# Kernel optimization log

Hardware: AMD Instinct MI355X
Metric: run time of the kernel (lower is better)

Reference implementation:

```python
import jax, jax.numpy as jnp
import numpy as np

# module config (init_kwargs + opts)
C = 64
RADIUS = 1.5          # radius in pixels
SIZE = 256            # square image size
K = 8                 # points_per_pixel (z-buffer depth)
RAD_POW = 2
TAU = 1.0


def setup_inputs() -> dict:
    key = jax.random.key(0)
    k1, k2 = jax.random.split(key)
    B, P = 2, 1024
    u = jax.random.uniform(k1, (B, P, 3), dtype=jnp.float32)
    xy = u[..., :2] * 2.0 - 1.0          # NDC xy in [-1, 1]
    z = u[..., 2:] * 1.9 + 0.1           # depth in [0.1, 2.0], in front of camera
    pts3D = jnp.concatenate([xy, z], axis=-1)
    src = jax.random.normal(k2, (B, C, P), dtype=jnp.float32)
    return {"pts3D": pts3D, "src": src}


def reference(pts3D, src):
    """Point rasterization (pytorch3d rasterize_points semantics for a square
    NDC image) + alpha-composite z-buffer blending, as in SynSin's
    RasterizePointsXYsBlending.forward (3-D src branch, alphacomposite)."""
    B, P, _ = pts3D.shape
    H = W = SIZE
    # module negates x and y before rasterizing (pytorch3d NDC: +x left, +y up)
    x = -pts3D[..., 0]                   # [B, P]
    y = -pts3D[..., 1]                   # [B, P]
    z = pts3D[..., 2]                    # [B, P]
    r_ndc = RADIUS / SIZE * 2.0          # radius in NDC units

    # pixel-center NDC coordinates
    xf = 1.0 - (2.0 * jnp.arange(W, dtype=pts3D.dtype) + 1.0) / W   # [W]
    yf = 1.0 - (2.0 * jnp.arange(H, dtype=pts3D.dtype) + 1.0) / H   # [H]

    dx2 = (xf[None, :, None] - x[:, None, :]) ** 2   # [B, W, P]
    dy2 = (yf[None, :, None] - y[:, None, :]) ** 2   # [B, H, P]
    dist2 = dy2[:, :, None, :] + dx2[:, None, :, :]  # [B, H, W, P] screen-space sq dist

    # a point covers a pixel if within radius and in front of the camera
    valid = (dist2 <= r_ndc * r_ndc) & (z[:, None, None, :] > 0.0)
    zkey = jnp.where(valid, z[:, None, None, :], jnp.inf)
    negz, idx = jax.lax.top_k(-zkey, K)              # K nearest in z, front-to-back
    sel_valid = jnp.isfinite(negz)                   # [B, H, W, K] (idx = -1 slots)

    dist_sel = jnp.take_along_axis(dist2, idx, axis=-1)   # [B, H, W, K]
    dist_n = dist_sel / (r_ndc ** RAD_POW)
    alphas = (1.0 - jnp.sqrt(jnp.clip(dist_n, 0.001, 1.0))) ** TAU
    alphas = jnp.where(sel_valid, alphas, 0.0)            # [B, H, W, K]

    # alpha compositing: w_k = a_k * prod_{j<k} (1 - a_j)
    one_m = 1.0 - alphas
    excl = jnp.concatenate(
        [jnp.ones_like(one_m[..., :1]), jnp.cumprod(one_m, axis=-1)[..., :-1]],
        axis=-1,
    )
    w = alphas * excl                                      # [B, H, W, K]

    feats = jnp.transpose(src, (0, 2, 1))                  # [B, P, C]
    idx_c = jnp.clip(idx, 0, P - 1).reshape(B, -1)         # [B, H*W*K]
    gathered = jnp.take_along_axis(feats, idx_c[..., None], axis=1)
    gathered = gathered.reshape(B, H, W, K, C)             # [B, H, W, K, C]

    out = jnp.einsum('bhwk,bhwkc->bchw', w, gathered)      # [B, C, H, W]
    return out
```

## Files before the change

kernel.cpp:

```cpp
#include <hip/hip_runtime.h>

#define NCH 64
#define IMG 256
#define KSEL 8
#define CAP 64
#define FPAD 17

__global__ __launch_bounds__(256) void raster_blend_kernel(
    const float* __restrict__ pts3D,
    const float* __restrict__ src,
    float* __restrict__ out,
    int P)
{
    const int h = blockIdx.x;
    const int b = blockIdx.y;
    const int w = threadIdx.x;
    const int HW = IMG * IMG;

    const float r_ndc  = (1.5f / (float)IMG) * 2.0f;
    const float r2     = r_ndc * r_ndc;
    const float inv_r2 = 1.0f / r2;

    const float yf = 1.0f - (2.0f * (float)h + 1.0f) / (float)IMG;
    const float xf = 1.0f - (2.0f * (float)w + 1.0f) / (float)IMG;

    __shared__ __align__(16) float4 cand[CAP];
    __shared__ int   cnt;
    __shared__ __align__(16) float featS[CAP * FPAD * 4];
    if (w == 0) cnt = 0;
    __syncthreads();

    const float* pb = pts3D + (size_t)b * P * 3;
    for (int p = w; p < P; p += 256) {
        float px = -pb[p * 3 + 0];
        float py = -pb[p * 3 + 1];
        float pz =  pb[p * 3 + 2];
        float dy = yf - py;
        if (dy * dy <= r2 && pz > 0.0f) {
            int slot = atomicAdd(&cnt, 1);
            if (slot < CAP)
                cand[slot] = make_float4(px, py, pz, __int_as_float(p));
        }
    }
    __syncthreads();
    const int n = min(cnt, CAP);

    const int myj = w >> 6;
    const int c   = w & 63;
    const float* sb = src + (size_t)b * NCH * P;
    int cidx[CAP / 4];
#pragma unroll
    for (int r = 0; r < CAP / 4; ++r) {
        int j = r * 4 + myj;
        if (j < n) cidx[r] = __float_as_int(cand[j].w);
    }
    float freg[CAP / 4];
#pragma unroll
    for (int r = 0; r < CAP / 4; ++r) {
        int j = r * 4 + myj;
        if (j < n) freg[r] = sb[(size_t)c * P + cidx[r]];
    }

    const float SENT = 1e30f;
    float zb[KSEL], db[KSEL];
    int   jb[KSEL];
#pragma unroll
    for (int s = 0; s < KSEL; ++s) { zb[s] = SENT; db[s] = 0.0f; jb[s] = 0; }

    for (int j = 0; j < n; ++j) {
        float4 e = cand[j];
        float dx = xf - e.x;
        float dy = yf - e.y;
        float d2 = fmaf(dx, dx, dy * dy);
        float z  = e.z;
        if (d2 <= r2 && z < zb[KSEL - 1]) {
            float carz = z, card = d2;
            int   carj = j;
#pragma unroll
            for (int s = 0; s < KSEL; ++s) {
                if (carz < zb[s]) {
                    float tz = zb[s]; zb[s] = carz; carz = tz;
                    float td = db[s]; db[s] = card; card = td;
                    int   tj = jb[s]; jb[s] = carj; carj = tj;
                }
            }
        }
    }

    float wk[KSEL];
    bool  vk[KSEL];
    float T = 1.0f;
#pragma unroll
    for (int s = 0; s < KSEL; ++s) {
        bool valid = zb[s] < 1e29f;
        vk[s] = valid;
        float dn = db[s] * inv_r2;
        dn = fminf(fmaxf(dn, 0.001f), 1.0f);
        float a = 1.0f - sqrtf(dn);
        a = valid ? a : 0.0f;
        wk[s] = a * T;
        T *= (1.0f - a);
    }

#pragma unroll
    for (int r = 0; r < CAP / 4; ++r) {
        int j = r * 4 + myj;
        if (j < n) featS[j * (FPAD * 4) + c] = freg[r];
    }
    __syncthreads();

    float4 acc[NCH / 4];
#pragma unroll
    for (int c4 = 0; c4 < NCH / 4; ++c4) acc[c4] = make_float4(0.f, 0.f, 0.f, 0.f);

    const float4* fv = (const float4*)featS;
#pragma unroll
    for (int k = 0; k < KSEL; ++k) {
        if (__any(vk[k])) {
            float wv = wk[k];
            const float4* fp = fv + jb[k] * FPAD;
#pragma unroll
            for (int c4 = 0; c4 < NCH / 4; ++c4) {
                float4 f = fp[c4];
                acc[c4].x = fmaf(wv, f.x, acc[c4].x);
                acc[c4].y = fmaf(wv, f.y, acc[c4].y);
                acc[c4].z = fmaf(wv, f.z, acc[c4].z);
                acc[c4].w = fmaf(wv, f.w, acc[c4].w);
            }
        }
    }

    float* op = out + (size_t)b * NCH * HW + (size_t)h * IMG + w;
#pragma unroll
    for (int c4 = 0; c4 < NCH / 4; ++c4) {
        op[(size_t)(4 * c4 + 0) * HW] = acc[c4].x;
        op[(size_t)(4 * c4 + 1) * HW] = acc[c4].y;
        op[(size_t)(4 * c4 + 2) * HW] = acc[c4].z;
        op[(size_t)(4 * c4 + 3) * HW] = acc[c4].w;
    }
}

extern "C" void kernel_launch(void* const* d_in, const int* in_sizes, int n_in,
                              void* d_out, int out_size, void* d_ws, size_t ws_size,
                              hipStream_t stream) {
    const float* pts3D = (const float*)d_in[0];
    const float* src   = (const float*)d_in[1];
    float* out = (float*)d_out;

    const int B = out_size / (NCH * IMG * IMG);
    const int P = in_sizes[0] / (3 * B);

    dim3 grid(IMG, B, 1);
    dim3 block(256, 1, 1);
    raster_blend_kernel<<<grid, block, 0, stream>>>(pts3D, src, out, P);
}
```

Before: 72.84 us.

## Split channels across grid z-dimension to cut registers and raise occupancy

Adds a third grid dimension that splits the 64 output channels into 4 groups of 16. Each block now gathers and accumulates only its 16 channels, which shrinks the accumulator and feature registers and the shared-memory feature tile, and launch bounds now request 4 blocks per CU. The cost is that each of the 4 blocks repeats the candidate scan and per-pixel z-sort, so that work is done four times. The composite loop also exits early once no lane has a valid slot.

After: 73.62 us. About the same (+1.1%).

```diff
diff --git a/kernel.cpp b/kernel.cpp
--- a/kernel.cpp
+++ b/kernel.cpp
@@ -4,9 +4,11 @@
 #define IMG 256
 #define KSEL 8
 #define CAP 64
-#define FPAD 17
+#define NG 4
+#define CG (NCH / NG)
+#define FSTR 5
 
-__global__ __launch_bounds__(256) void raster_blend_kernel(
+__global__ __launch_bounds__(256, 4) void raster_blend_kernel(
     const float* __restrict__ pts3D,
     const float* __restrict__ src,
     float* __restrict__ out,
@@ -14,6 +16,7 @@
 {
     const int h = blockIdx.x;
     const int b = blockIdx.y;
+    const int g = blockIdx.z;
     const int w = threadIdx.x;
     const int HW = IMG * IMG;
 
@@ -25,8 +28,8 @@
     const float xf = 1.0f - (2.0f * (float)w + 1.0f) / (float)IMG;
 
     __shared__ __align__(16) float4 cand[CAP];
-    __shared__ int   cnt;
-    __shared__ __align__(16) float featS[CAP * FPAD * 4];
+    __shared__ int cnt;
+    __shared__ __align__(16) float4 featS[CAP * FSTR];
     if (w == 0) cnt = 0;
     __syncthreads();
 
@@ -45,20 +48,20 @@
     __syncthreads();
     const int n = min(cnt, CAP);
 
-    const int myj = w >> 6;
-    const int c   = w & 63;
-    const float* sb = src + (size_t)b * NCH * P;
-    int cidx[CAP / 4];
+    const int jr = w >> 4;
+    const int cc = w & 15;
+    const float* sb = src + ((size_t)b * NCH + (size_t)(g * CG + cc)) * P;
+    int   cidx[CAP / 16];
+    float freg[CAP / 16];
 #pragma unroll
-    for (int r = 0; r < CAP / 4; ++r) {
-        int j = r * 4 + myj;
+    for (int r = 0; r < CAP / 16; ++r) {
+        int j = r * 16 + jr;
         if (j < n) cidx[r] = __float_as_int(cand[j].w);
     }
-    float freg[CAP / 4];
 #pragma unroll
-    for (int r = 0; r < CAP / 4; ++r) {
-        int j = r * 4 + myj;
-        if (j < n) freg[r] = sb[(size_t)c * P + cidx[r]];
+    for (int r = 0; r < CAP / 16; ++r) {
+        int j = r * 16 + jr;
+        if (j < n) freg[r] = sb[cidx[r]];
     }
 
     const float SENT = 1e30f;
@@ -88,12 +91,10 @@
     }
 
     float wk[KSEL];
-    bool  vk[KSEL];
     float T = 1.0f;
 #pragma unroll
     for (int s = 0; s < KSEL; ++s) {
         bool valid = zb[s] < 1e29f;
-        vk[s] = valid;
         float dn = db[s] * inv_r2;
         dn = fminf(fmaxf(dn, 0.001f), 1.0f);
         float a = 1.0f - sqrtf(dn);
@@ -102,37 +103,37 @@
         T *= (1.0f - a);
     }
 
+    float* fS = (float*)featS;
 #pragma unroll
-    for (int r = 0; r < CAP / 4; ++r) {
-        int j = r * 4 + myj;
-        if (j < n) featS[j * (FPAD * 4) + c] = freg[r];
+    for (int r = 0; r < CAP / 16; ++r) {
+        int j = r * 16 + jr;
+        if (j < n) fS[j * (FSTR * 4) + cc] = freg[r];
     }
     __syncthreads();
 
-    float4 acc[NCH / 4];
+    float4 acc[CG / 4];
 #pragma unroll
-    for (int c4 = 0; c4 < NCH / 4; ++c4) acc[c4] = make_float4(0.f, 0.f, 0.f, 0.f);
+    for (int c4 = 0; c4 < CG / 4; ++c4) acc[c4] = make_float4(0.f, 0.f, 0.f, 0.f);
 
-    const float4* fv = (const float4*)featS;
+    const float4* fv = featS;
 #pragma unroll
     for (int k = 0; k < KSEL; ++k) {
-        if (__any(vk[k])) {
-            float wv = wk[k];
-            const float4* fp = fv + jb[k] * FPAD;
+        if (!__any(zb[k] < 1e29f)) break;
+        float wv = wk[k];
+        const float4* fp = fv + (size_t)jb[k] * FSTR;
 #pragma unroll
-            for (int c4 = 0; c4 < NCH / 4; ++c4) {
-                float4 f = fp[c4];
-                acc[c4].x = fmaf(wv, f.x, acc[c4].x);
-                acc[c4].y = fmaf(wv, f.y, acc[c4].y);
-                acc[c4].z = fmaf(wv, f.z, acc[c4].z);
-                acc[c4].w = fmaf(wv, f.w, acc[c4].w);
-            }
+        for (int c4 = 0; c4 < CG / 4; ++c4) {
+            float4 f = fp[c4];
+            acc[c4].x = fmaf(wv, f.x, acc[c4].x);
+            acc[c4].y = fmaf(wv, f.y, acc[c4].y);
+            acc[c4].z = fmaf(wv, f.z, acc[c4].z);
+            acc[c4].w = fmaf(wv, f.w, acc[c4].w);
         }
     }
 
-    float* op = out + (size_t)b * NCH * HW + (size_t)h * IMG + w;
+    float* op = out + ((size_t)b * NCH + (size_t)(g * CG)) * HW + (size_t)h * IMG + w;
 #pragma unroll
-    for (int c4 = 0; c4 < NCH / 4; ++c4) {
+    for (int c4 = 0; c4 < CG / 4; ++c4) {
         op[(size_t)(4 * c4 + 0) * HW] = acc[c4].x;
         op[(size_t)(4 * c4 + 1) * HW] = acc[c4].y;
         op[(size_t)(4 * c4 + 2) * HW] = acc[c4].z;
@@ -150,7 +151,7 @@
     const int B = out_size / (NCH * IMG * IMG);
     const int P = in_sizes[0] / (3 * B);
 
-    dim3 grid(IMG, B, 1);
+    dim3 grid(IMG, B, NG);
     dim3 block(256, 1, 1);
     raster_blend_kernel<<<grid, block, 0, stream>>>(pts3D, src, out, P);
 }
```
